# Kernel tuning notes

Hardware: AMD Instinct MI355X
Metric: run time of the kernel (lower is better)

Reference implementation:

```python
import jax, jax.numpy as jnp
import numpy as np

B, T, D, H, C = 32, 512, 768, 512, 7


def setup_inputs() -> dict:
    key = jax.random.key(0)
    ks = jax.random.split(key, 10)
    g = lambda k, shape: jax.random.normal(k, shape, jnp.float32) * 0.02
    return {
        "x": jax.random.normal(ks[0], (B, T, D), jnp.float32),
        # PyTorch LSTM params; b = b_ih + b_hh folded into one bias (same math)
        "Wf_ih": g(ks[1], (4 * H, 2 * D)),
        "Wf_hh": g(ks[2], (4 * H, H)),
        "bf": jnp.zeros((4 * H,), jnp.float32),
        "Wb_ih": g(ks[3], (4 * H, 2 * D)),
        "Wb_hh": g(ks[4], (4 * H, H)),
        "bb": jnp.zeros((4 * H,), jnp.float32),
        "W_enc": g(ks[5], (H, D)),
        "b_enc": jnp.zeros((H,), jnp.float32),
        "W_dec": g(ks[6], (H, H)),
        "b_dec": jnp.zeros((H,), jnp.float32),
        "v": jax.random.uniform(ks[7], (H,), jnpp := jnp.float32) if False else jax.random.uniform(ks[7], (H,), jnp.float32),
        "W_head": g(ks[8], (C, 2 * H)),
        "b_head": jnp.zeros((C,), jnp.float32),
    }


def reference(x, Wf_ih, Wf_hh, bf, Wb_ih, Wb_hh, bb, W_enc, b_enc, W_dec, b_dec, v, W_head, b_head):
    hid = W_dec.shape[0]
    # encoder projection is time-invariant -> hoist out of the loop (same math as original)
    enc_proj = jnp.einsum('btd,hd->bth', x, W_enc) + b_enc  # (B,T,H)

    def run_direction(x_seq, Wih, Whh, b):
        def step(carry, xt):
            h, c = carry                                    # (B,H) each
            dec = h @ W_dec.T + b_dec                       # (B,H)
            scores = jnp.tanh(enc_proj + dec[:, None, :]) @ v  # (B,T)
            w = jax.nn.softmax(scores, axis=1)
            ctx = jnp.einsum('bt,btd->bd', w, x)            # (B,D)
            inp = jnp.concatenate([ctx, xt], axis=1)        # (B,2D)
            gates = inp @ Wih.T + h @ Whh.T + b             # (B,4H), torch order i,f,g,o
            i_, f_, g_, o_ = jnp.split(gates, 4, axis=1)
            c = jax.nn.sigmoid(f_) * c + jax.nn.sigmoid(i_) * jnp.tanh(g_)
            h = jax.nn.sigmoid(o_) * jnp.tanh(c)
            return (h, c), h

        h0 = jnp.zeros((x.shape[0], hid), x.dtype)
        (_, _), hs = jax.lax.scan(step, (h0, h0), x_seq)
        return hs                                           # (T,B,H)

    x_seq = jnp.swapaxes(x, 0, 1)                           # (T,B,D)
    hs_f = run_direction(x_seq, Wf_ih, Wf_hh, bf)
    hs_b = run_direction(x_seq[::-1], Wb_ih, Wb_hh, bb)[::-1]
    comb = jnp.swapaxes(jnp.concatenate([hs_f, hs_b], axis=-1), 0, 1)  # (B,T,2H)
    return comb @ W_head.T + b_head                          # (B,T,C)
```

## Files before the change

kernel.cpp:

```cpp
#include <hip/hip_runtime.h>
#include <cstdint>
#include <cstddef>

#define L2E 1.4426950408889634f

typedef __attribute__((ext_vector_type(8))) short short8v;
typedef __attribute__((ext_vector_type(4))) float f32x4;
typedef unsigned long long ull;

__device__ __forceinline__ float fexp2(float x){ return __builtin_amdgcn_exp2f(x); }
__device__ __forceinline__ float frcp(float x){ return __builtin_amdgcn_rcpf(x); }
__device__ __forceinline__ float tanh_f(float x){
  return 1.f - 2.f*frcp(1.f + fexp2(2.f*L2E*x));
}
__device__ __forceinline__ float sigm_f(float x){
  return frcp(1.f + fexp2(-L2E*x));
}
__device__ __forceinline__ float bf2f(ushort u){ return __uint_as_float(((uint32_t)u)<<16); }
__device__ __forceinline__ ushort f2bf(float f){
  uint32_t x = __float_as_uint(f);
  uint32_t r = (x + 0x7FFFu + ((x>>16)&1u)) >> 16;
  return (ushort)r;
}

__device__ __forceinline__ float ld4f(const float* p){
  return __hip_atomic_load((float*)p, __ATOMIC_RELAXED, __HIP_MEMORY_SCOPE_AGENT);
}
__device__ __forceinline__ void st4f(float* p, float v){
  __hip_atomic_store(p, v, __ATOMIC_RELAXED, __HIP_MEMORY_SCOPE_AGENT);
}
__device__ __forceinline__ void st2h(ushort* p, ushort v){
  __hip_atomic_store(p, v, __ATOMIC_RELAXED, __HIP_MEMORY_SCOPE_AGENT);
}
__device__ __forceinline__ short8v ld16h(const ushort* p){
  union { ull u[2]; short8v s; } c;
  c.u[0] = __hip_atomic_load((ull*)p,     __ATOMIC_RELAXED, __HIP_MEMORY_SCOPE_AGENT);
  c.u[1] = __hip_atomic_load((ull*)(p+4), __ATOMIC_RELAXED, __HIP_MEMORY_SCOPE_AGENT);
  return c.s;
}
__device__ __forceinline__ void st8u(ushort* p, ull v){
  __hip_atomic_store((ull*)p, v, __ATOMIC_RELAXED, __HIP_MEMORY_SCOPE_AGENT);
}

namespace {
constexpr int NB = 32, TT = 512, DD = 768, HH = 512;
constexpr size_t EPB  = 0;
constexpr size_t XBB  = EPB  + (size_t)NB*HH*TT*2;
constexpr size_t HSB  = XBB  + (size_t)NB*TT*DD*2;
constexpr size_t WPKB = HSB  + (size_t)2*TT*NB*HH*2;
constexpr size_t WDPB = WPKB + (size_t)2*128*64*64*8*2;
constexpr size_t CTXB = WDPB + (size_t)32*16*64*8*2;
constexpr size_t EVGB = CTXB + (size_t)2*NB*DD*4;
constexpr size_t CSTB = EVGB + (size_t)NB*2*512*4;
constexpr size_t GSYB = CSTB + (size_t)2*NB*HH*4;
constexpr size_t WS_BYTES = GSYB + 49152;

constexpr int EPL  = 0;
constexpr int WPL  = 65536;
constexpr int REDL = 131072;
constexpr int HEVL = 147456;
constexpr int HBL  = 151680;
constexpr int DPL  = 153856;
constexpr int DECL = 155904;
constexpr int VVL  = 156416;
constexpr int CSCL = 156672;
constexpr int GFNL = 159776;
constexpr int LDS_BYTES = GFNL + 2176;
}

__device__ __forceinline__ void bar_arrive(uint* flags, uint token, int bid){
  __syncthreads();
  if (threadIdx.x == 0)
    __hip_atomic_store(&flags[bid*16], token, __ATOMIC_RELAXED, __HIP_MEMORY_SCOPE_AGENT);
}
__device__ __forceinline__ void bar_wait(uint* flags, uint token){
  if (threadIdx.x < 256) {
    while (__hip_atomic_load(&flags[threadIdx.x*16], __ATOMIC_RELAXED, __HIP_MEMORY_SCOPE_AGENT) < token)
      __builtin_amdgcn_s_sleep(1);
  }
  __syncthreads();
  asm volatile("" ::: "memory");
}

__global__ void k_xcast(const float* __restrict__ x, ushort* __restrict__ xb)
{
  size_t i = ((size_t)blockIdx.x*256 + threadIdx.x)*8;
  float4 v0 = *(const float4*)(x + i);
  float4 v1 = *(const float4*)(x + i + 4);
  short8v o;
  o[0]=(short)f2bf(v0.x); o[1]=(short)f2bf(v0.y); o[2]=(short)f2bf(v0.z); o[3]=(short)f2bf(v0.w);
  o[4]=(short)f2bf(v1.x); o[5]=(short)f2bf(v1.y); o[6]=(short)f2bf(v1.z); o[7]=(short)f2bf(v1.w);
  *(short8v*)(xb + i) = o;
}

__global__ void k_encproj(const float* __restrict__ x, const float* __restrict__ Wenc,
                          const float* __restrict__ benc, ushort* __restrict__ epT)
{
  int b = blockIdx.z, h0 = blockIdx.y*64, t0 = blockIdx.x*64;
  __shared__ float As[64][33];
  __shared__ float Bs[64][33];
  int tid = threadIdx.x;
  int n = tid & 63, mg = tid >> 6;
  float acc[16];
  #pragma unroll
  for (int j = 0; j < 16; j++) acc[j] = 0.f;
  int lr = tid >> 2, lk = (tid & 3) * 8;
  for (int k0 = 0; k0 < 768; k0 += 32) {
    const float* ap = Wenc + (size_t)(h0 + lr)*768 + k0 + lk;
    #pragma unroll
    for (int i = 0; i < 8; i++) As[lr][lk + i] = ap[i];
    const float* bp = x + ((size_t)b*512 + t0 + lr)*768 + k0 + lk;
    #pragma unroll
    for (int i = 0; i < 8; i++) Bs[lr][lk + i] = bp[i];
    __syncthreads();
    #pragma unroll
    for (int kk = 0; kk < 32; kk++) {
      float bv = Bs[n][kk];
      #pragma unroll
      for (int j = 0; j < 16; j++) acc[j] += As[mg*16 + j][kk] * bv;
    }
    __syncthreads();
  }
  #pragma unroll
  for (int j = 0; j < 16; j++) {
    int h = h0 + mg*16 + j;
    epT[((size_t)b*512 + h)*512 + t0 + n] = f2bf(acc[j] + benc[h]);
  }
}

__global__ void k_wpack(const float* __restrict__ Wfih, const float* __restrict__ Wfhh,
                        const float* __restrict__ Wbih, const float* __restrict__ Wbhh,
                        ushort* __restrict__ wpk)
{
  size_t f = (size_t)blockIdx.x*256 + threadIdx.x;
  int lane = (int)(f & 63), kstep = (int)((f>>6)&63), jblk = (int)((f>>12)&127), dir = (int)(f>>19);
  const float* Whh = dir ? Wbhh : Wfhh;
  const float* Wih = dir ? Wbih : Wfih;
  int c = lane & 15, gate = c >> 2, jj = c & 3;
  int row = gate*512 + jblk*4 + jj;
  int kbase = kstep*32 + (lane>>4)*8;
  short8v o;
  #pragma unroll
  for (int i = 0; i < 8; i++) {
    int k = kbase + i;
    float w = (k < 512) ? Whh[(size_t)row*512 + k] : Wih[(size_t)row*1536 + (k - 512)];
    o[i] = (short)f2bf(w);
  }
  *(short8v*)(wpk + f*8) = o;
}

__global__ void k_wdpack(const float* __restrict__ Wdec, ushort* __restrict__ wdp)
{
  int f = blockIdx.x*256 + threadIdx.x;
  int lane = f & 63, kstep = (f >> 6) & 15, nb = f >> 10;
  int n = nb*16 + (lane & 15);
  int kbase = kstep*32 + (lane >> 4)*8;
  short8v o;
  #pragma unroll
  for (int i = 0; i < 8; i++) o[i] = (short)f2bf(Wdec[(size_t)n*512 + kbase + i]);
  *(short8v*)(wdp + (size_t)f*8) = o;
}

__device__ __forceinline__ void gates_hx(int s, int wid, int lane, int l15, int lk8, int dirG,
    const ushort* __restrict__ hsb, const ushort* __restrict__ xb,
    const ushort* wpk_l, float* RED)
{
  if (wid >= 2 && wid <= 4) return;
  int b0 = l15, b1 = 16 + l15;
  f32x4 acc0 = {0,0,0,0}, acc1 = {0,0,0,0};
  if (wid < 2) {
    if (s > 0) {
      int t_prev = dirG ? (512 - s) : (s - 1);
      const ushort* h0 = hsb + (((size_t)dirG*512 + t_prev)*32 + b0)*512;
      const ushort* h1 = hsb + (((size_t)dirG*512 + t_prev)*32 + b1)*512;
      #pragma unroll
      for (int kk = 0; kk < 8; kk++) {
        int kstep = wid*8 + kk;
        int ko = kstep*32 + lk8;
        short8v a0v = *(const short8v*)(h0 + ko);
        short8v a1v = *(const short8v*)(h1 + ko);
        short8v bv  = *(const short8v*)(wpk_l + (size_t)kstep*512 + lane*8);
        acc0 = __builtin_amdgcn_mfma_f32_16x16x32_bf16(a0v, bv, acc0, 0, 0, 0);
        acc1 = __builtin_amdgcn_mfma_f32_16x16x32_bf16(a1v, bv, acc1, 0, 0, 0);
      }
    }
  } else {
    int t_in = dirG ? (511 - s) : s;
    const ushort* x0 = xb + ((size_t)b0*512 + t_in)*768;
    const ushort* x1 = xb + ((size_t)b1*512 + t_in)*768;
    #pragma unroll
    for (int kk = 0; kk < 8; kk++) {
      int kstep = wid*8 + kk;
      int ko = kstep*32 - 1280 + lk8;
      short8v a0v = *(const short8v*)(x0 + ko);
      short8v a1v = *(const short8v*)(x1 + ko);
      short8v bv  = *(const short8v*)(wpk_l + (size_t)kstep*512 + lane*8);
      acc0 = __builtin_amdgcn_mfma_f32_16x16x32_bf16(a0v, bv, acc0, 0, 0, 0);
      acc1 = __builtin_amdgcn_mfma_f32_16x16x32_bf16(a1v, bv, acc1, 0, 0, 0);
    }
  }
  int rr = (lane >> 4) * 4;
  #pragma unroll
  for (int r = 0; r < 4; r++) RED[((size_t)wid*32 + rr + r)*16 + l15] = acc0[r];
  #pragma unroll
  for (int r = 0; r < 4; r++) RED[((size_t)wid*32 + 16 + rr + r)*16 + l15] = acc1[r];
}

__global__ __launch_bounds__(512, 1) void k_loop(
    ushort* __restrict__ hsb, const ushort* __restrict__ xb, const ushort* __restrict__ ep,
    const ushort* __restrict__ wpk, const ushort* __restrict__ wdp,
    float* __restrict__ spart, ushort* __restrict__ ctxf, float* __restrict__ evt_g,
    float* __restrict__ cst, const float* __restrict__ bdec, const float* __restrict__ vg,
    const float* __restrict__ bfv, const float* __restrict__ bbv,
    uint* __restrict__ flags, uint* __restrict__ gfl, uint* __restrict__ gfl2)
{
  extern __shared__ __align__(16) char dsm[];
  ushort* ep_l  = (ushort*)(dsm + EPL);
  ushort* wpk_l = (ushort*)(dsm + WPL);
  float*  RED   = (float*)(dsm + REDL);
  float*  HEV   = (float*)(dsm + HEVL);
  ushort* HB    = (ushort*)(dsm + HBL);
  float*  DP    = (float*)(dsm + DPL);
  float*  DEC   = (float*)(dsm + DECL);
  float*  VV    = (float*)(dsm + VVL);
  float*  CSC   = (float*)(dsm + CSCL);
  float*  GFIN  = (float*)(dsm + GFNL);

  const int bid = blockIdx.x;
  const int tid = threadIdx.x;
  const int wid = tid >> 6, lane = tid & 63;
  const int l15 = lane & 15, lk8 = (lane >> 4) * 8;
  const int bS = bid >> 3, hc = bid & 7;
  const int dirG = bid >> 7, jblkG = bid & 127;
  uint bar_t = 0;

  {
    const short8v* esrc = (const short8v*)(ep + ((size_t)bS*512 + hc*64)*512);
    short8v* edst = (short8v*)ep_l;
    for (int i = tid; i < 4096; i += 512) edst[i] = esrc[i];
    const short8v* wsrc = (const short8v*)(wpk + (((size_t)dirG*128 + jblkG)*64)*512);
    short8v* wdst = (short8v*)wpk_l;
    for (int i = tid; i < 4096; i += 512) wdst[i] = wsrc[i];
    if (tid < 64) VV[tid] = vg[hc*64 + tid];
  }
  ++bar_t; bar_arrive(flags, bar_t, bid); bar_wait(flags, bar_t);

  for (int s = 0; s < TT; ++s) {
    if (s == 0) {
      if (tid < 128) { int dir = tid >> 6, n = tid & 63; DEC[dir*64 + n] = bdec[hc*64 + n]; }
    } else {
      if (tid < 128) {
        int dir = tid >> 6, q = tid & 63;
        int tp = dir ? (512 - s) : (s - 1);
        short8v hv = *(const short8v*)(hsb + (((size_t)dir*512 + tp)*32 + bS)*512 + q*8);
        *(short8v*)&HB[(dir*4 + (q >> 4))*136 + (q & 15)*8] = hv;
      }
      __syncthreads();
      {
        int dir = tid >> 8, n = (tid >> 2) & 63, kq = tid & 3;
        int ng = hc*64 + n, nb = ng >> 4, c = ng & 15;
        const ushort* hrow = HB + (dir*4 + kq)*136;
        float a = 0.f;
        #pragma unroll
        for (int ch = 0; ch < 16; ch++) {
          int kstep = kq*4 + (ch >> 2), lhi = ch & 3;
          short8v w8 = *(const short8v*)(wdp + (((size_t)nb*16 + kstep)*64 + lhi*16 + c)*8);
          #pragma unroll
          for (int j = 0; j < 8; j++) a += bf2f((ushort)w8[j]) * bf2f(hrow[ch*8 + j]);
        }
        DP[tid] = a;
      }
      __syncthreads();
      if (tid < 128) {
        int dir = tid >> 6, n = tid & 63;
        const float* dp = DP + dir*256 + n*4;
        DEC[dir*64 + n] = dp[0] + dp[1] + dp[2] + dp[3] + bdec[hc*64 + n];
      }
    }
    __syncthreads();

    float s0 = 0.f, s1 = 0.f;
    {
      int t = tid;
      #pragma unroll 8
      for (int h = 0; h < 64; h++) {
        float e = bf2f(ep_l[h*512 + t]);
        float vv = VV[h];
        s0 += tanh_f(e + DEC[h]) * vv;
        s1 += tanh_f(e + DEC[64 + h]) * vv;
      }
    }

    if (hc != 0) {
      float* sp = spart + (((size_t)(bS*8 + hc))*2)*512;
      st4f(sp + tid, s0);
      st4f(sp + 512 + tid, s1);
      __syncthreads();
      if (tid == 0)
        __hip_atomic_store(&gfl[bid*16], (uint)(s + 1), __ATOMIC_RELAXED, __HIP_MEMORY_SCOPE_AGENT);
      gates_hx(s, wid, lane, l15, lk8, dirG, hsb, xb, wpk_l, RED);
      if (tid == 0) {
        while (__hip_atomic_load(&gfl2[bS*16], __ATOMIC_RELAXED, __HIP_MEMORY_SCOPE_AGENT) < (uint)(s + 1))
          __builtin_amdgcn_s_sleep(1);
      }
      __syncthreads();
      {
        float e0 = ld4f(evt_g + (size_t)bS*1024 + tid);
        float e1 = ld4f(evt_g + (size_t)bS*1024 + 512 + tid);
        HEV[(tid >> 7)*132 + (tid & 127)] = e0;
        HEV[(4 + (tid >> 7))*132 + (tid & 127)] = e1;
      }
      __syncthreads();
    } else {
      if (tid >= 1 && tid < 8) {
        while (__hip_atomic_load(&gfl[(bS*8 + tid)*16], __ATOMIC_RELAXED, __HIP_MEMORY_SCOPE_AGENT) < (uint)(s + 1))
          __builtin_amdgcn_s_sleep(1);
      }
      __syncthreads();
      float s0r = s0, s1r = s1;
      #pragma unroll
      for (int j = 1; j < 8; j++) {
        const float* sp = spart + (((size_t)(bS*8 + j))*2)*512;
        s0r += ld4f(sp + tid);
        s1r += ld4f(sp + 512 + tid);
      }
      s0r = fminf(s0r, 100.f); s1r = fminf(s1r, 100.f);
      float e0 = fexp2((s0r - 32.f)*L2E);
      float e1 = fexp2((s1r - 32.f)*L2E);
      float z0 = e0, z1 = e1;
      #pragma unroll
      for (int off = 32; off; off >>= 1) { z0 += __shfl_xor(z0, off); z1 += __shfl_xor(z1, off); }
      if (lane == 0) { DP[wid] = z0; DP[8 + wid] = z1; }
      __syncthreads();
      if (tid < 2) {
        float z = 0.f;
        #pragma unroll
        for (int w = 0; w < 8; w++) z += DP[tid*8 + w];
        DP[128 + tid] = frcp(z);
      }
      __syncthreads();
      e0 *= DP[128]; e1 *= DP[129];
      HEV[(tid >> 7)*132 + (tid & 127)] = e0;
      HEV[(4 + (tid >> 7))*132 + (tid & 127)] = e1;
      st4f(evt_g + (size_t)bS*1024 + tid, e0);
      st4f(evt_g + (size_t)bS*1024 + 512 + tid, e1);
      __syncthreads();
      if (tid == 0)
        __hip_atomic_store(&gfl2[bS*16], (uint)(s + 1), __ATOMIC_RELAXED, __HIP_MEMORY_SCOPE_AGENT);
    }

    if (tid < 384) {
      int dl = tid % 96, tq = tid / 96;
      const ushort* xp = xb + (((size_t)bS*512 + tq*128)*768) + hc*96 + dl;
      const float* ev0 = HEV + tq*132;
      const float* ev1 = HEV + (4 + tq)*132;
      float a0 = 0.f, a1 = 0.f;
      #pragma unroll 8
      for (int t2 = 0; t2 < 128; t2++) {
        float xv = bf2f(xp[(size_t)t2*768]);
        a0 += ev0[t2]*xv;
        a1 += ev1[t2]*xv;
      }
      CSC[(tq*2 + 0)*97 + dl] = a0;
      CSC[(tq*2 + 1)*97 + dl] = a1;
    }
    __syncthreads();
    if (tid < 192) {
      int dl = tid % 96, dir = tid / 96;
      float cv = CSC[(0*2 + dir)*97 + dl] + CSC[(1*2 + dir)*97 + dl]
               + CSC[(2*2 + dir)*97 + dl] + CSC[(3*2 + dir)*97 + dl];
      st2h(ctxf + ((size_t)dir*32 + bS)*768 + hc*96 + dl, f2bf(cv));
    }

    ++bar_t; bar_arrive(flags, bar_t, bid);
    if (hc == 0) gates_hx(s, wid, lane, l15, lk8, dirG, hsb, xb, wpk_l, RED);
    bar_wait(flags, bar_t);

    {
      if (wid >= 2 && wid <= 4) {
        int b0 = l15, b1 = 16 + l15;
        f32x4 acc0 = {0,0,0,0}, acc1 = {0,0,0,0};
        const ushort* c0 = ctxf + ((size_t)dirG*32 + b0)*768;
        const ushort* c1 = ctxf + ((size_t)dirG*32 + b1)*768;
        #pragma unroll
        for (int kk = 0; kk < 8; kk++) {
          int kstep = wid*8 + kk;
          int ko = kstep*32 - 512 + lk8;
          short8v a0v = ld16h(c0 + ko);
          short8v a1v = ld16h(c1 + ko);
          short8v bv  = *(const short8v*)(wpk_l + (size_t)kstep*512 + lane*8);
          acc0 = __builtin_amdgcn_mfma_f32_16x16x32_bf16(a0v, bv, acc0, 0, 0, 0);
          acc1 = __builtin_amdgcn_mfma_f32_16x16x32_bf16(a1v, bv, acc1, 0, 0, 0);
        }
        int rr = (lane >> 4) * 4;
        #pragma unroll
        for (int r = 0; r < 4; r++) RED[((size_t)wid*32 + rr + r)*16 + l15] = acc0[r];
        #pragma unroll
        for (int r = 0; r < 4; r++) RED[((size_t)wid*32 + 16 + rr + r)*16 + l15] = acc1[r];
      }
      __syncthreads();
      {
        int bb = tid >> 4, c = tid & 15;
        float g = 0.f;
        #pragma unroll
        for (int w = 0; w < 8; w++) g += RED[((size_t)w*32 + bb)*16 + c];
        GFIN[bb*17 + c] = g;
      }
      __syncthreads();
      if (tid < 32) {
        int b = tid;
        int j0 = jblkG*4;
        const float* bias = dirG ? bbv : bfv;
        size_t ci0 = ((size_t)dirG*32 + b)*512 + j0;
        float4 co = *(const float4*)&cst[ci0];
        float cold[4] = {co.x, co.y, co.z, co.w};
        float4 cn4;
        ull hp = 0;
        #pragma unroll
        for (int jj = 0; jj < 4; jj++) {
          int j = j0 + jj;
          float gi  = GFIN[b*17 + jj]       + bias[j];
          float gf  = GFIN[b*17 + 4 + jj]   + bias[512 + j];
          float gg  = GFIN[b*17 + 8 + jj]   + bias[1024 + j];
          float go_ = GFIN[b*17 + 12 + jj]  + bias[1536 + j];
          float cn = sigm_f(gf)*cold[jj] + sigm_f(gi)*tanh_f(gg);
          float h  = sigm_f(go_)*tanh_f(cn);
          ((float*)&cn4)[jj] = cn;
          hp |= ((ull)f2bf(h)) << (16*jj);
        }
        *(float4*)&cst[ci0] = cn4;
        int tw = dirG ? (511 - s) : s;
        st8u(hsb + (((size_t)dirG*512 + tw)*32 + b)*512 + j0, hp);
      }
    }
    ++bar_t; bar_arrive(flags, bar_t, bid);
    bar_wait(flags, bar_t);
  }
}

__global__ void k_head(const ushort* __restrict__ hsb, const float* __restrict__ Wh,
                       const float* __restrict__ bh, float* __restrict__ out)
{
  int wid = threadIdx.x >> 6, lane = threadIdx.x & 63;
  int r = blockIdx.x*4 + wid;
  int b = r >> 9, t = r & 511;
  float acc[7];
  #pragma unroll
  for (int c = 0; c < 7; c++) acc[c] = 0.f;
  const ushort* hf = hsb + (((size_t)t)*32 + b)*512;
  const ushort* hb = hsb + (((size_t)512 + t)*32 + b)*512;
  for (int k0 = 0; k0 < 512; k0 += 64) {
    int k = k0 + lane;
    float a = bf2f(hf[k]), bvv = bf2f(hb[k]);
    #pragma unroll
    for (int c = 0; c < 7; c++)
      acc[c] += a*Wh[c*1024 + k] + bvv*Wh[c*1024 + 512 + k];
  }
  #pragma unroll
  for (int c = 0; c < 7; c++) {
    float sres = acc[c];
    #pragma unroll
    for (int off = 32; off; off >>= 1) sres += __shfl_xor(sres, off);
    if (lane == c) out[((size_t)b*512 + t)*7 + c] = sres + bh[c];
  }
}

extern "C" void kernel_launch(void* const* d_in, const int* in_sizes, int n_in,
                              void* d_out, int out_size, void* d_ws, size_t ws_size,
                              hipStream_t stream) {
  (void)in_sizes; (void)n_in; (void)out_size;
  const float* x    = (const float*)d_in[0];
  const float* Wfih = (const float*)d_in[1];
  const float* Wfhh = (const float*)d_in[2];
  const float* bfv  = (const float*)d_in[3];
  const float* Wbih = (const float*)d_in[4];
  const float* Wbhh = (const float*)d_in[5];
  const float* bbv  = (const float*)d_in[6];
  const float* Wenc = (const float*)d_in[7];
  const float* benc = (const float*)d_in[8];
  const float* Wdec = (const float*)d_in[9];
  const float* bdec = (const float*)d_in[10];
  const float* v    = (const float*)d_in[11];
  const float* Whead= (const float*)d_in[12];
  const float* bhead= (const float*)d_in[13];
  float* out = (float*)d_out;
  char* ws = (char*)d_ws;

  if (ws_size < WS_BYTES) return;

  ushort* ep   = (ushort*)(ws + EPB);
  float*  spart= (float*)(ws + EPB);
  ushort* xb   = (ushort*)(ws + XBB);
  ushort* hsb  = (ushort*)(ws + HSB);
  ushort* wpk  = (ushort*)(ws + WPKB);
  ushort* wdp  = (ushort*)(ws + WDPB);
  ushort* ctxf = (ushort*)(ws + CTXB);
  float*  evtg = (float*)(ws + EVGB);
  float*  cst  = (float*)(ws + CSTB);
  uint*   flags= (uint*)(ws + GSYB);
  uint*   gfl  = (uint*)(ws + GSYB + 16384);
  uint*   gfl2 = (uint*)(ws + GSYB + 32768);

  hipFuncSetAttribute(reinterpret_cast<const void*>(k_loop),
                      hipFuncAttributeMaxDynamicSharedMemorySize, LDS_BYTES);

  hipMemsetAsync(ws + CSTB, 0, (size_t)2*NB*HH*4, stream);
  hipMemsetAsync(ws + GSYB, 0, 49152, stream);

  hipLaunchKernelGGL(k_xcast, dim3(6144), dim3(256), 0, stream, x, xb);
  hipLaunchKernelGGL(k_encproj, dim3(8,8,32), dim3(256), 0, stream, x, Wenc, benc, ep);
  hipLaunchKernelGGL(k_wpack, dim3(4096), dim3(256), 0, stream, Wfih, Wfhh, Wbih, Wbhh, wpk);
  hipLaunchKernelGGL(k_wdpack, dim3(128), dim3(256), 0, stream, Wdec, wdp);

  void* args[] = {
    (void*)&hsb, (void*)&xb, (void*)&ep, (void*)&wpk, (void*)&wdp,
    (void*)&spart, (void*)&ctxf, (void*)&evtg, (void*)&cst,
    (void*)&bdec, (void*)&v, (void*)&bfv, (void*)&bbv,
    (void*)&flags, (void*)&gfl, (void*)&gfl2
  };
  hipLaunchCooperativeKernel(reinterpret_cast<void*>(k_loop), dim3(256), dim3(512),
                             args, LDS_BYTES, stream);

  hipLaunchKernelGGL(k_head, dim3(4096), dim3(256), 0, stream, hsb, Whead, bhead, out);
}
```

Before: 13.60 ms.

## Prefetch next step's input-gate MFMA into the end-of-step barrier wait

Splits the fused h/x gate contribution into separate gates_h and gates_x routines. The x-part, which depends only on the input sequence, is now computed for step s+1 between the barrier arrive and wait at the end of step s, and for step 0 before the loop. This moves work off the per-step critical path and hides it behind grid-barrier latency. It depends on the RED slots for waves 5-7 not being overwritten between the prefetch and their later use.

```diff
diff --git a/kernel.cpp b/kernel.cpp
--- a/kernel.cpp
+++ b/kernel.cpp
@@ -161,43 +161,52 @@
   *(short8v*)(wdp + (size_t)f*8) = o;
 }
 
-__device__ __forceinline__ void gates_hx(int s, int wid, int lane, int l15, int lk8, int dirG,
-    const ushort* __restrict__ hsb, const ushort* __restrict__ xb,
-    const ushort* wpk_l, float* RED)
-{
-  if (wid >= 2 && wid <= 4) return;
+__device__ __forceinline__ void gates_h(int s, int wid, int lane, int l15, int lk8, int dirG,
+    const ushort* __restrict__ hsb, const ushort* wpk_l, float* RED)
+{
+  if (wid >= 2) return;
   int b0 = l15, b1 = 16 + l15;
   f32x4 acc0 = {0,0,0,0}, acc1 = {0,0,0,0};
-  if (wid < 2) {
-    if (s > 0) {
-      int t_prev = dirG ? (512 - s) : (s - 1);
-      const ushort* h0 = hsb + (((size_t)dirG*512 + t_prev)*32 + b0)*512;
-      const ushort* h1 = hsb + (((size_t)dirG*512 + t_prev)*32 + b1)*512;
-      #pragma unroll
-      for (int kk = 0; kk < 8; kk++) {
-        int kstep = wid*8 + kk;
-        int ko = kstep*32 + lk8;
-        short8v a0v = *(const short8v*)(h0 + ko);
-        short8v a1v = *(const short8v*)(h1 + ko);
-        short8v bv  = *(const short8v*)(wpk_l + (size_t)kstep*512 + lane*8);
-        acc0 = __builtin_amdgcn_mfma_f32_16x16x32_bf16(a0v, bv, acc0, 0, 0, 0);
-        acc1 = __builtin_amdgcn_mfma_f32_16x16x32_bf16(a1v, bv, acc1, 0, 0, 0);
-      }
-    }
-  } else {
-    int t_in = dirG ? (511 - s) : s;
-    const ushort* x0 = xb + ((size_t)b0*512 + t_in)*768;
-    const ushort* x1 = xb + ((size_t)b1*512 + t_in)*768;
+  if (s > 0) {
+    int t_prev = dirG ? (512 - s) : (s - 1);
+    const ushort* h0 = hsb + (((size_t)dirG*512 + t_prev)*32 + b0)*512;
+    const ushort* h1 = hsb + (((size_t)dirG*512 + t_prev)*32 + b1)*512;
     #pragma unroll
     for (int kk = 0; kk < 8; kk++) {
       int kstep = wid*8 + kk;
-      int ko = kstep*32 - 1280 + lk8;
-      short8v a0v = *(const short8v*)(x0 + ko);
-      short8v a1v = *(const short8v*)(x1 + ko);
+      int ko = kstep*32 + lk8;
+      short8v a0v = *(const short8v*)(h0 + ko);
+      short8v a1v = *(const short8v*)(h1 + ko);
       short8v bv  = *(const short8v*)(wpk_l + (size_t)kstep*512 + lane*8);
       acc0 = __builtin_amdgcn_mfma_f32_16x16x32_bf16(a0v, bv, acc0, 0, 0, 0);
       acc1 = __builtin_amdgcn_mfma_f32_16x16x32_bf16(a1v, bv, acc1, 0, 0, 0);
     }
+  }
+  int rr = (lane >> 4) * 4;
+  #pragma unroll
+  for (int r = 0; r < 4; r++) RED[((size_t)wid*32 + rr + r)*16 + l15] = acc0[r];
+  #pragma unroll
+  for (int r = 0; r < 4; r++) RED[((size_t)wid*32 + 16 + rr + r)*16 + l15] = acc1[r];
+}
+
+__device__ __forceinline__ void gates_x(int s, int wid, int lane, int l15, int lk8, int dirG,
+    const ushort* __restrict__ xb, const ushort* wpk_l, float* RED)
+{
+  if (wid < 5) return;
+  int b0 = l15, b1 = 16 + l15;
+  f32x4 acc0 = {0,0,0,0}, acc1 = {0,0,0,0};
+  int t_in = dirG ? (511 - s) : s;
+  const ushort* x0 = xb + ((size_t)b0*512 + t_in)*768;
+  const ushort* x1 = xb + ((size_t)b1*512 + t_in)*768;
+  #pragma unroll
+  for (int kk = 0; kk < 8; kk++) {
+    int kstep = wid*8 + kk;
+    int ko = kstep*32 - 1280 + lk8;
+    short8v a0v = *(const short8v*)(x0 + ko);
+    short8v a1v = *(const short8v*)(x1 + ko);
+    short8v bv  = *(const short8v*)(wpk_l + (size_t)kstep*512 + lane*8);
+    acc0 = __builtin_amdgcn_mfma_f32_16x16x32_bf16(a0v, bv, acc0, 0, 0, 0);
+    acc1 = __builtin_amdgcn_mfma_f32_16x16x32_bf16(a1v, bv, acc1, 0, 0, 0);
   }
   int rr = (lane >> 4) * 4;
   #pragma unroll
@@ -243,7 +252,9 @@
     for (int i = tid; i < 4096; i += 512) wdst[i] = wsrc[i];
     if (tid < 64) VV[tid] = vg[hc*64 + tid];
   }
-  ++bar_t; bar_arrive(flags, bar_t, bid); bar_wait(flags, bar_t);
+  ++bar_t; bar_arrive(flags, bar_t, bid);
+  gates_x(0, wid, lane, l15, lk8, dirG, xb, wpk_l, RED);
+  bar_wait(flags, bar_t);
 
   for (int s = 0; s < TT; ++s) {
     if (s == 0) {
@@ -298,7 +309,7 @@
       __syncthreads();
       if (tid == 0)
         __hip_atomic_store(&gfl[bid*16], (uint)(s + 1), __ATOMIC_RELAXED, __HIP_MEMORY_SCOPE_AGENT);
-      gates_hx(s, wid, lane, l15, lk8, dirG, hsb, xb, wpk_l, RED);
+      gates_h(s, wid, lane, l15, lk8, dirG, hsb, wpk_l, RED);
       if (tid == 0) {
         while (__hip_atomic_load(&gfl2[bS*16], __ATOMIC_RELAXED, __HIP_MEMORY_SCOPE_AGENT) < (uint)(s + 1))
           __builtin_amdgcn_s_sleep(1);
@@ -373,7 +384,7 @@
     }
 
     ++bar_t; bar_arrive(flags, bar_t, bid);
-    if (hc == 0) gates_hx(s, wid, lane, l15, lk8, dirG, hsb, xb, wpk_l, RED);
+    if (hc == 0) gates_h(s, wid, lane, l15, lk8, dirG, hsb, wpk_l, RED);
     bar_wait(flags, bar_t);
 
     {
@@ -434,6 +445,8 @@
       }
     }
     ++bar_t; bar_arrive(flags, bar_t, bid);
+    if (s + 1 < TT)
+      gates_x(s + 1, wid, lane, l15, lk8, dirG, xb, wpk_l, RED);
     bar_wait(flags, bar_t);
   }
 }
```

New measurement: 13.99 ms. 2.8% more time.
